# Kernel optimization log

Hardware: AMD Instinct MI355X
Metric: run time of the kernel (lower is better)

## Reference

```python
import jax, jax.numpy as jnp
import numpy as np

B, CIN, COUT, H, W = 2, 128, 128, 128, 256
KH, KW = 3, 3
CMID = 32  # COUT // low_factor


def setup_inputs() -> dict:
    key = jax.random.key(0)
    ks = jax.random.split(key, 7)
    x = jax.random.normal(ks[0], (B, CIN, H, W), jnp.float32)
    # torchvision deform_conv2d offset layout: [2*KH*KW, Ho, Wo], (dy, dx) per tap
    offset = jax.random.normal(ks[1], (2 * KH * KW, H, W), jnp.float32)
    weight = jax.random.normal(ks[2], (COUT, CIN, KH, KW), jnp.float32) * 0.05
    bias = jax.random.normal(ks[3], (COUT,), jnp.float32) * 0.01
    down_w = jax.random.normal(ks[4], (CMID, 2 * COUT), jnp.float32) * 0.05
    up_w = jax.random.normal(ks[5], (COUT, CMID), jnp.float32) * 0.05
    scale = jnp.float32(1.0)
    return dict(x=x, offset=offset, weight=weight, bias=bias,
                down_w=down_w, up_w=up_w, scale=scale)


def _deform_conv2d(x, offset, weight, bias):
    # stride=1, padding=1, dilation=1, groups=1 (matches init_conv config)
    Bn, C, Hh, Ww = x.shape
    Co, _, kh, kw = weight.shape
    K = kh * kw
    Ho, Wo = offset.shape[-2:]
    off = offset.reshape(K, 2, Ho, Wo)
    dy, dx = off[:, 0], off[:, 1]                      # [K, Ho, Wo]
    ki, kj = jnp.meshgrid(jnp.arange(kh), jnp.arange(kw), indexing='ij')
    ki = ki.reshape(K).astype(jnp.float32)
    kj = kj.reshape(K).astype(jnp.float32)
    i = jnp.arange(Ho, dtype=jnp.float32)
    j = jnp.arange(Wo, dtype=jnp.float32)
    PAD = 1.0
    py = i[None, :, None] - PAD + ki[:, None, None] + dy   # [K, Ho, Wo]
    px = j[None, None, :] - PAD + kj[:, None, None] + dx
    y0 = jnp.floor(py).astype(jnp.int32)
    x0 = jnp.floor(px).astype(jnp.int32)
    fy = py - y0.astype(py.dtype)
    fx = px - x0.astype(px.dtype)
    xf = x.reshape(Bn, C, Hh * Ww)

    def gather(yi, xi, w):
        # zero padding outside the image (torchvision semantics)
        valid = (yi >= 0) & (yi < Hh) & (xi >= 0) & (xi < Ww)
        yc = jnp.clip(yi, 0, Hh - 1)
        xc = jnp.clip(xi, 0, Ww - 1)
        idx = (yc * Ww + xc).reshape(-1)                   # [K*Ho*Wo]
        g = xf[:, :, idx].reshape(Bn, C, K, Ho, Wo)
        return g * (w * valid.astype(w.dtype))[None, None]

    val = gather(y0, x0, (1.0 - fy) * (1.0 - fx))
    val = val + gather(y0, x0 + 1, (1.0 - fy) * fx)
    val = val + gather(y0 + 1, x0, fy * (1.0 - fx))
    val = val + gather(y0 + 1, x0 + 1, fy * fx)
    out = jnp.einsum('bcnij,ocn->boij', val, weight.reshape(Co, C, K))
    return out + bias[None, :, None, None]


def reference(x, offset, weight, bias, down_w, up_w, scale):
    # h = original frozen conv (weights shared with the deform branch, ablation != wo_copy)
    h = jax.lax.conv_general_dilated(
        x, weight, window_strides=(1, 1), padding=[(1, 1), (1, 1)],
        dimension_numbers=('NCHW', 'OIHW', 'NCHW'))
    h = h + bias[None, :, None, None]
    dx = _deform_conv2d(x, offset, weight, bias)
    dx = jnp.concatenate([dx, h], axis=1)                  # mix == 'cat'
    lo = jnp.einsum('bcij,dc->bdij', dx, down_w)           # 1x1 conv_down
    up = jnp.einsum('bcij,dc->bdij', lo, up_w)             # 1x1 conv_up
    return h + scale * up
```

## Files before the change

kernel.cpp:

```cpp
#include <hip/hip_runtime.h>
#include <hip/hip_bf16.h>

typedef __attribute__((ext_vector_type(8))) short short8;
typedef __attribute__((ext_vector_type(8))) unsigned short ushort8;
typedef __attribute__((ext_vector_type(4))) float f32x4;
typedef __attribute__((ext_vector_type(4))) int int4v;
typedef __attribute__((ext_vector_type(4))) float float4v;
typedef __attribute__((ext_vector_type(2))) float float2v;
typedef __attribute__((ext_vector_type(4))) unsigned int uint4v;

#define HH 128
#define WW 256
#define CIN_ 128
#define COUT_ 128

__device__ __forceinline__ float bf2f(unsigned short u) {
  return __builtin_bit_cast(float, ((unsigned int)u) << 16);
}
__device__ __forceinline__ unsigned short f2bf(float f) {
  union { __hip_bfloat16 h; unsigned short u; } v;
  v.h = __float2bfloat16(f);
  return v.u;
}

__global__ void k_prep_T(const float* __restrict__ down_w,
                         const float* __restrict__ weight,
                         float* __restrict__ T) {
  int e = blockIdx.x * 256 + threadIdx.x;
  if (e >= 2 * 32 * 1152) return;
  int s = e / 36864, r = e % 36864, d = r / 1152, ck = r % 1152;
  float a = 0.f;
  #pragma unroll 4
  for (int p = 0; p < 128; ++p)
    a += down_w[d * 256 + s * 128 + p] * weight[p * 1152 + ck];
  T[e] = a;
}

__global__ void k_prep_W(const float* __restrict__ up_w,
                         const float* __restrict__ weight,
                         const float* __restrict__ T,
                         const float* __restrict__ scale,
                         unsigned short* __restrict__ wdef,
                         unsigned short* __restrict__ wstd) {
  int e = blockIdx.x * 256 + threadIdx.x;
  if (e >= 2 * 9 * 128 * 128) return;
  int s = e / 147456, r = e % 147456;
  int tap = r / 16384, o = (r / 128) % 128, c = r % 128;
  int ck = c * 9 + tap;
  const float* Ts = T + s * 36864;
  float a = 0.f;
  #pragma unroll
  for (int d = 0; d < 32; ++d) a += up_w[o * 32 + d] * Ts[d * 1152 + ck];
  float scl = scale[0];
  int idx = ((tap * 4 + (c >> 5)) * 128 + o) * 32 + (c & 31);
  if (s == 1) {
    wstd[idx] = f2bf(weight[o * 1152 + ck] + scl * a);
  } else {
    wdef[idx] = f2bf(scl * a);
  }
}

__global__ void k_prep_bias(const float* __restrict__ down_w,
                            const float* __restrict__ up_w,
                            const float* __restrict__ bias,
                            const float* __restrict__ scale,
                            float* __restrict__ beff) {
  __shared__ float sd[32];
  int t = threadIdx.x;
  if (t < 32) {
    float a = 0.f;
    for (int p = 0; p < 128; ++p)
      a += (down_w[t * 256 + p] + down_w[t * 256 + 128 + p]) * bias[p];
    sd[t] = a;
  }
  __syncthreads();
  if (t < 128) {
    float a = 0.f;
    #pragma unroll
    for (int d = 0; d < 32; ++d) a += up_w[t * 32 + d] * sd[d];
    beff[t] = bias[t] + scale[0] * a;
  }
}

__global__ __launch_bounds__(256) void k_nhwc(const float* __restrict__ x,
                                              unsigned short* __restrict__ xh) {
  __shared__ float tile[32 * 129];
  int idx = blockIdx.x;
  int b = idx >> 10, rem = idx & 1023;
  int y = rem >> 3, xg = (rem & 7) << 5;
  int tid = threadIdx.x;
  for (int it = tid; it < 32 * 128; it += 256) {
    int c = it >> 5, xi = it & 31;
    tile[xi * 129 + c] = x[(((size_t)b * 128 + c) * 128 + y) * 256 + xg + xi];
  }
  __syncthreads();
  for (int it = tid; it < 32 * 16; it += 256) {
    int xi = it >> 4, cs = it & 15;
    ushort8 v;
    #pragma unroll
    for (int e = 0; e < 8; ++e) v[e] = f2bf(tile[xi * 129 + cs * 8 + e]);
    *(ushort8*)(xh + (((size_t)b * 128 + y) * 256 + xg + xi) * 128 + cs * 8) = v;
  }
}

__global__ void k_meta(const float* __restrict__ offset,
                       int4v* __restrict__ mo, float4v* __restrict__ mw) {
  int e = blockIdx.x * 256 + threadIdx.x;
  if (e >= 9 * 128 * 256) return;
  int k = e >> 15, rem = e & 32767;
  int ii = rem >> 8, jj = rem & 255;
  float dy = offset[(2 * k) * 32768 + rem];
  float dx = offset[(2 * k + 1) * 32768 + rem];
  int ki = k / 3, kj = k % 3;
  float py = (float)(ii - 1 + ki) + dy;
  float px = (float)(jj - 1 + kj) + dx;
  float fy0 = floorf(py), fx0 = floorf(px);
  int y0 = (int)fy0, x0 = (int)fx0;
  float fy = py - fy0, fx = px - fx0;
  int ys[2] = {y0, y0 + 1};
  int xs_[2] = {x0, x0 + 1};
  float wy[2] = {1.f - fy, fy}, wx[2] = {1.f - fx, fx};
  int4v o;
  float4v w;
  #pragma unroll
  for (int cy = 0; cy < 2; ++cy) {
    #pragma unroll
    for (int cx = 0; cx < 2; ++cx) {
      int yy = ys[cy], xx = xs_[cx];
      bool valid = (yy >= 0) && (yy < HH) && (xx >= 0) && (xx < WW);
      int yc = min(max(yy, 0), HH - 1), xc = min(max(xx, 0), WW - 1);
      int off = (yc * WW + xc) * CIN_;
      float wv = valid ? wy[cy] * wx[cx] : 0.f;
      int ci = cy * 2 + cx;
      if (ci == 0) { o.x = off; w.x = wv; }
      else if (ci == 1) { o.y = off; w.y = wv; }
      else if (ci == 2) { o.z = off; w.z = wv; }
      else { o.w = off; w.w = wv; }
    }
  }
  mo[e] = o;
  mw[e] = w;
}

__global__ __launch_bounds__(256, 4) void k_main(
    const unsigned short* __restrict__ xh,
    const int4v* __restrict__ mo, const float4v* __restrict__ mw,
    const unsigned short* __restrict__ wstd, const unsigned short* __restrict__ wdef,
    const float* __restrict__ beff, float* __restrict__ out) {
  __shared__ __align__(16) unsigned short sbuf[2][64 * 128];

  int t = blockIdx.x;
  int b = t >> 9, i = (t >> 2) & 127, j0 = (t & 3) << 6;
  int tid = threadIdx.x;
  const unsigned short* xb = xh + (size_t)b * (HH * WW * CIN_);

  int slot = tid & 15, pg = tid >> 4;
  int ce = slot * 8;

  int lane = tid & 63, wid = tid >> 6;
  int obase = wid << 5;
  int lrow = lane & 15, lhi = lane >> 4;

  f32x4 acc[2][4] = {};

  auto STAGE_DEF = [&](int tap, unsigned short* buf) {
    int4v o;
    float4v wq0, wq1;
    uint4v g0[4], g1[4];
    int mbase = (tap * HH + i) * WW + j0 + pg;

    o = mo[mbase]; wq0 = mw[mbase];
    g0[0] = *(const uint4v*)(xb + o.x + ce);
    g0[1] = *(const uint4v*)(xb + o.y + ce);
    g0[2] = *(const uint4v*)(xb + o.z + ce);
    g0[3] = *(const uint4v*)(xb + o.w + ce);
    o = mo[mbase + 16]; wq1 = mw[mbase + 16];
    g1[0] = *(const uint4v*)(xb + o.x + ce);
    g1[1] = *(const uint4v*)(xb + o.y + ce);
    g1[2] = *(const uint4v*)(xb + o.z + ce);
    g1[3] = *(const uint4v*)(xb + o.w + ce);

    auto COMB = [&](uint4v* g, float4v w, int q) {
      int p = q * 16 + pg;
      uint4v r;
      #pragma unroll
      for (int wi = 0; wi < 4; ++wi) {
        unsigned u0 = g[0][wi], u1 = g[1][wi], u2 = g[2][wi], u3 = g[3][wi];
        float2v f0 = {__builtin_bit_cast(float, u0 << 16), __builtin_bit_cast(float, u0 & 0xffff0000u)};
        float2v f1 = {__builtin_bit_cast(float, u1 << 16), __builtin_bit_cast(float, u1 & 0xffff0000u)};
        float2v f2 = {__builtin_bit_cast(float, u2 << 16), __builtin_bit_cast(float, u2 & 0xffff0000u)};
        float2v f3 = {__builtin_bit_cast(float, u3 << 16), __builtin_bit_cast(float, u3 & 0xffff0000u)};
        float2v s = w.x * f0 + w.y * f1 + w.z * f2 + w.w * f3;
        r[wi] = (unsigned)f2bf(s.x) | ((unsigned)f2bf(s.y) << 16);
      }
      *(uint4v*)((char*)buf + (p << 8) + ((slot ^ (p & 15)) << 4)) = r;
    };

    COMB(g0, wq0, 0);
    o = mo[mbase + 32]; wq0 = mw[mbase + 32];
    g0[0] = *(const uint4v*)(xb + o.x + ce);
    g0[1] = *(const uint4v*)(xb + o.y + ce);
    g0[2] = *(const uint4v*)(xb + o.z + ce);
    g0[3] = *(const uint4v*)(xb + o.w + ce);
    COMB(g1, wq1, 1);
    o = mo[mbase + 48]; wq1 = mw[mbase + 48];
    g1[0] = *(const uint4v*)(xb + o.x + ce);
    g1[1] = *(const uint4v*)(xb + o.y + ce);
    g1[2] = *(const uint4v*)(xb + o.z + ce);
    g1[3] = *(const uint4v*)(xb + o.w + ce);
    COMB(g0, wq0, 2);
    COMB(g1, wq1, 3);
  };

  auto STAGE_STD = [&](int tap, unsigned short* buf) {
    int ki = tap / 3, kj = tap % 3;
    int gy = i - 1 + ki;
    bool oky = (unsigned)gy < (unsigned)HH;
    uint4v s[4];
    #pragma unroll
    for (int q = 0; q < 4; ++q) {
      int p = q * 16 + pg;
      int gx = j0 + p - 1 + kj;
      uint4v vv = {};
      if (oky && (unsigned)gx < (unsigned)WW)
        vv = *(const uint4v*)(xb + (size_t)(gy * WW + gx) * CIN_ + ce);
      s[q] = vv;
    }
    #pragma unroll
    for (int q = 0; q < 4; ++q) {
      int p = q * 16 + pg;
      *(uint4v*)((char*)buf + (p << 8) + ((slot ^ (p & 15)) << 4)) = s[q];
    }
  };

  auto COMPUTE = [&](int v) {
    const unsigned short* cur = sbuf[v & 1];
    const unsigned short* wt = ((v & 1) ? wdef : wstd) + (size_t)(v >> 1) * 16384;
    #pragma unroll
    for (int cc = 0; cc < 4; ++cc) {
      short8 af[2];
      #pragma unroll
      for (int am = 0; am < 2; ++am)
        af[am] = *(const short8*)(wt + ((size_t)(cc * 128 + obase + am * 16 + lrow)) * 32 + lhi * 8);
      short8 bfr[4];
      #pragma unroll
      for (int bn = 0; bn < 4; ++bn) {
        int pp = bn * 16 + lrow;
        bfr[bn] = *(const short8*)((const char*)cur + (pp << 8) +
                                   (((cc * 4 + lhi) ^ lrow) << 4));
      }
      #pragma unroll
      for (int am = 0; am < 2; ++am)
        #pragma unroll
        for (int bn = 0; bn < 4; ++bn)
          acc[am][bn] = __builtin_amdgcn_mfma_f32_16x16x32_bf16(af[am], bfr[bn], acc[am][bn], 0, 0, 0);
    }
  };

  STAGE_STD(0, sbuf[0]);
  __syncthreads();

  for (int v = 0; v < 18; ++v) {
    if (v < 17) {
      int nv = v + 1;
      if (nv & 1) STAGE_DEF(nv >> 1, sbuf[nv & 1]);
      else        STAGE_STD(nv >> 1, sbuf[nv & 1]);
    }
    COMPUTE(v);
    __syncthreads();
  }

  #pragma unroll
  for (int am = 0; am < 2; ++am) {
    #pragma unroll
    for (int bn = 0; bn < 4; ++bn) {
      int jg = j0 + bn * 16 + lrow;
      #pragma unroll
      for (int r = 0; r < 4; ++r) {
        int o = obase + am * 16 + lhi * 4 + r;
        out[(((size_t)b * COUT_ + o) * HH + i) * WW + jg] = acc[am][bn][r] + beff[o];
      }
    }
  }
}

extern "C" void kernel_launch(void* const* d_in, const int* in_sizes, int n_in,
                              void* d_out, int out_size, void* d_ws, size_t ws_size,
                              hipStream_t stream) {
  const float* x      = (const float*)d_in[0];
  const float* offset = (const float*)d_in[1];
  const float* weight = (const float*)d_in[2];
  const float* bias   = (const float*)d_in[3];
  const float* down_w = (const float*)d_in[4];
  const float* up_w   = (const float*)d_in[5];
  const float* scale  = (const float*)d_in[6];
  float* out = (float*)d_out;

  char* ws = (char*)d_ws;
  unsigned short* xh   = (unsigned short*)(ws);
  int4v* mo            = (int4v*)(ws + 16777216);
  float4v* mw          = (float4v*)(ws + 21495808);
  unsigned short* wstd = (unsigned short*)(ws + 26214400);
  unsigned short* wdef = (unsigned short*)(ws + 26509312);
  float* T             = (float*)(ws + 26804224);
  float* beff          = (float*)(ws + 27099136);

  k_prep_T<<<dim3(288), dim3(256), 0, stream>>>(down_w, weight, T);
  k_prep_W<<<dim3(1152), dim3(256), 0, stream>>>(up_w, weight, T, scale, wdef, wstd);
  k_prep_bias<<<dim3(1), dim3(128), 0, stream>>>(down_w, up_w, bias, scale, beff);
  k_nhwc<<<dim3(2048), dim3(256), 0, stream>>>(x, xh);
  k_meta<<<dim3(1152), dim3(256), 0, stream>>>(offset, mo, mw);
  k_main<<<dim3(1024), dim3(256), 0, stream>>>(xh, mo, mw, wstd, wdef, beff, out);
}
```

Measured before the change: 115.1 us.

## Interleave gather loads with split MFMA compute and remap block order

```diff
diff --git a/kernel.cpp b/kernel.cpp
--- a/kernel.cpp
+++ b/kernel.cpp
@@ -127,7 +127,7 @@
     #pragma unroll
     for (int cx = 0; cx < 2; ++cx) {
       int yy = ys[cy], xx = xs_[cx];
-      bool valid = (yy >= 0) && (yy < HH) && (xx >= 0) && (xx < WW);
+      bool valid = (yy >= 0) && (yy < HH) && (xx < WW) && (xx >= 0);
       int yc = min(max(yy, 0), HH - 1), xc = min(max(xx, 0), WW - 1);
       int off = (yc * WW + xc) * CIN_;
       float wv = valid ? wy[cy] * wx[cx] : 0.f;
@@ -149,7 +149,8 @@
     const float* __restrict__ beff, float* __restrict__ out) {
   __shared__ __align__(16) unsigned short sbuf[2][64 * 128];
 
-  int t = blockIdx.x;
+  int orig = blockIdx.x;
+  int t = ((orig & 7) << 7) + (orig >> 3);
   int b = t >> 9, i = (t >> 2) & 127, j0 = (t & 3) << 6;
   int tid = threadIdx.x;
   const unsigned short* xb = xh + (size_t)b * (HH * WW * CIN_);
@@ -163,56 +164,25 @@
 
   f32x4 acc[2][4] = {};
 
-  auto STAGE_DEF = [&](int tap, unsigned short* buf) {
-    int4v o;
-    float4v wq0, wq1;
-    uint4v g0[4], g1[4];
-    int mbase = (tap * HH + i) * WW + j0 + pg;
-
-    o = mo[mbase]; wq0 = mw[mbase];
-    g0[0] = *(const uint4v*)(xb + o.x + ce);
-    g0[1] = *(const uint4v*)(xb + o.y + ce);
-    g0[2] = *(const uint4v*)(xb + o.z + ce);
-    g0[3] = *(const uint4v*)(xb + o.w + ce);
-    o = mo[mbase + 16]; wq1 = mw[mbase + 16];
-    g1[0] = *(const uint4v*)(xb + o.x + ce);
-    g1[1] = *(const uint4v*)(xb + o.y + ce);
-    g1[2] = *(const uint4v*)(xb + o.z + ce);
-    g1[3] = *(const uint4v*)(xb + o.w + ce);
-
-    auto COMB = [&](uint4v* g, float4v w, int q) {
-      int p = q * 16 + pg;
-      uint4v r;
-      #pragma unroll
-      for (int wi = 0; wi < 4; ++wi) {
-        unsigned u0 = g[0][wi], u1 = g[1][wi], u2 = g[2][wi], u3 = g[3][wi];
-        float2v f0 = {__builtin_bit_cast(float, u0 << 16), __builtin_bit_cast(float, u0 & 0xffff0000u)};
-        float2v f1 = {__builtin_bit_cast(float, u1 << 16), __builtin_bit_cast(float, u1 & 0xffff0000u)};
-        float2v f2 = {__builtin_bit_cast(float, u2 << 16), __builtin_bit_cast(float, u2 & 0xffff0000u)};
-        float2v f3 = {__builtin_bit_cast(float, u3 << 16), __builtin_bit_cast(float, u3 & 0xffff0000u)};
-        float2v s = w.x * f0 + w.y * f1 + w.z * f2 + w.w * f3;
-        r[wi] = (unsigned)f2bf(s.x) | ((unsigned)f2bf(s.y) << 16);
-      }
-      *(uint4v*)((char*)buf + (p << 8) + ((slot ^ (p & 15)) << 4)) = r;
-    };
-
-    COMB(g0, wq0, 0);
-    o = mo[mbase + 32]; wq0 = mw[mbase + 32];
-    g0[0] = *(const uint4v*)(xb + o.x + ce);
-    g0[1] = *(const uint4v*)(xb + o.y + ce);
-    g0[2] = *(const uint4v*)(xb + o.z + ce);
-    g0[3] = *(const uint4v*)(xb + o.w + ce);
-    COMB(g1, wq1, 1);
-    o = mo[mbase + 48]; wq1 = mw[mbase + 48];
-    g1[0] = *(const uint4v*)(xb + o.x + ce);
-    g1[1] = *(const uint4v*)(xb + o.y + ce);
-    g1[2] = *(const uint4v*)(xb + o.z + ce);
-    g1[3] = *(const uint4v*)(xb + o.w + ce);
-    COMB(g0, wq0, 2);
-    COMB(g1, wq1, 3);
+  auto COMB = [&](uint4v* g, float4v w, int q, unsigned short* buf) {
+    int p = q * 16 + pg;
+    uint4v r;
+    #pragma unroll
+    for (int wi = 0; wi < 4; ++wi) {
+      unsigned u0 = g[0][wi], u1 = g[1][wi], u2 = g[2][wi], u3 = g[3][wi];
+      float2v f0 = {__builtin_bit_cast(float, u0 << 16), __builtin_bit_cast(float, u0 & 0xffff0000u)};
+      float2v f1 = {__builtin_bit_cast(float, u1 << 16), __builtin_bit_cast(float, u1 & 0xffff0000u)};
+      float2v f2 = {__builtin_bit_cast(float, u2 << 16), __builtin_bit_cast(float, u2 & 0xffff0000u)};
+      float2v f3 = {__builtin_bit_cast(float, u3 << 16), __builtin_bit_cast(float, u3 & 0xffff0000u)};
+      float2v s = w.x * f0 + w.y * f1 + w.z * f2 + w.w * f3;
+      unsigned rr;
+      asm("v_cvt_pk_bf16_f32 %0, %1, %2" : "=v"(rr) : "v"(s.x), "v"(s.y));
+      r[wi] = rr;
+    }
+    *(uint4v*)((char*)buf + (p << 8) + ((slot ^ (p & 15)) << 4)) = r;
   };
 
-  auto STAGE_STD = [&](int tap, unsigned short* buf) {
+  auto STAGE_STD_FULL = [&](int tap, unsigned short* buf) {
     int ki = tap / 3, kj = tap % 3;
     int gy = i - 1 + ki;
     bool oky = (unsigned)gy < (unsigned)HH;
@@ -233,11 +203,12 @@
     }
   };
 
-  auto COMPUTE = [&](int v) {
+  auto COMPUTE_HALF = [&](int v, int half) {
     const unsigned short* cur = sbuf[v & 1];
     const unsigned short* wt = ((v & 1) ? wdef : wstd) + (size_t)(v >> 1) * 16384;
     #pragma unroll
-    for (int cc = 0; cc < 4; ++cc) {
+    for (int c2 = 0; c2 < 2; ++c2) {
+      int cc = half * 2 + c2;
       short8 af[2];
       #pragma unroll
       for (int am = 0; am < 2; ++am)
@@ -257,16 +228,83 @@
     }
   };
 
-  STAGE_STD(0, sbuf[0]);
+  STAGE_STD_FULL(0, sbuf[0]);
   __syncthreads();
 
   for (int v = 0; v < 18; ++v) {
-    if (v < 17) {
-      int nv = v + 1;
-      if (nv & 1) STAGE_DEF(nv >> 1, sbuf[nv & 1]);
-      else        STAGE_STD(nv >> 1, sbuf[nv & 1]);
-    }
-    COMPUTE(v);
+    int nv = v + 1;
+    if (nv < 18 && (nv & 1)) {
+      int tap = nv >> 1;
+      unsigned short* nb = sbuf[nv & 1];
+      int mbase = (tap * HH + i) * WW + j0 + pg;
+      int4v o0 = mo[mbase], o1 = mo[mbase + 16];
+      float4v w0 = mw[mbase], w1 = mw[mbase + 16];
+      uint4v gA[4], gB[4];
+      gA[0] = *(const uint4v*)(xb + o0.x + ce);
+      gA[1] = *(const uint4v*)(xb + o0.y + ce);
+      gA[2] = *(const uint4v*)(xb + o0.z + ce);
+      gA[3] = *(const uint4v*)(xb + o0.w + ce);
+      gB[0] = *(const uint4v*)(xb + o1.x + ce);
+      gB[1] = *(const uint4v*)(xb + o1.y + ce);
+      gB[2] = *(const uint4v*)(xb + o1.z + ce);
+      gB[3] = *(const uint4v*)(xb + o1.w + ce);
+      __builtin_amdgcn_sched_barrier(0);
+      COMPUTE_HALF(v, 0);
+      __builtin_amdgcn_sched_barrier(0);
+      COMB(gA, w0, 0, nb);
+      int4v o2 = mo[mbase + 32];
+      float4v w2 = mw[mbase + 32];
+      gA[0] = *(const uint4v*)(xb + o2.x + ce);
+      gA[1] = *(const uint4v*)(xb + o2.y + ce);
+      gA[2] = *(const uint4v*)(xb + o2.z + ce);
+      gA[3] = *(const uint4v*)(xb + o2.w + ce);
+      COMB(gB, w1, 1, nb);
+      int4v o3 = mo[mbase + 48];
+      float4v w3 = mw[mbase + 48];
+      gB[0] = *(const uint4v*)(xb + o3.x + ce);
+      gB[1] = *(const uint4v*)(xb + o3.y + ce);
+      gB[2] = *(const uint4v*)(xb + o3.z + ce);
+      gB[3] = *(const uint4v*)(xb + o3.w + ce);
+      __builtin_amdgcn_sched_barrier(0);
+      COMPUTE_HALF(v, 1);
+      __builtin_amdgcn_sched_barrier(0);
+      COMB(gA, w2, 2, nb);
+      COMB(gB, w3, 3, nb);
+    } else if (nv < 18) {
+      int tap = nv >> 1;
+      unsigned short* nb = sbuf[nv & 1];
+      int ki = tap / 3, kj = tap % 3;
+      int gy = i - 1 + ki;
+      bool oky = (unsigned)gy < (unsigned)HH;
+      uint4v s0 = {}, s1 = {}, s2 = {}, s3 = {};
+      {
+        int gx0 = j0 + pg - 1 + kj;
+        int gx1 = gx0 + 16, gx2 = gx0 + 32, gx3 = gx0 + 48;
+        if (oky && (unsigned)gx0 < (unsigned)WW)
+          s0 = *(const uint4v*)(xb + (size_t)(gy * WW + gx0) * CIN_ + ce);
+        if (oky && (unsigned)gx1 < (unsigned)WW)
+          s1 = *(const uint4v*)(xb + (size_t)(gy * WW + gx1) * CIN_ + ce);
+        if (oky && (unsigned)gx2 < (unsigned)WW)
+          s2 = *(const uint4v*)(xb + (size_t)(gy * WW + gx2) * CIN_ + ce);
+        if (oky && (unsigned)gx3 < (unsigned)WW)
+          s3 = *(const uint4v*)(xb + (size_t)(gy * WW + gx3) * CIN_ + ce);
+      }
+      __builtin_amdgcn_sched_barrier(0);
+      COMPUTE_HALF(v, 0);
+      __builtin_amdgcn_sched_barrier(0);
+      {
+        int p0 = pg, p1 = pg + 16, p2 = pg + 32, p3 = pg + 48;
+        *(uint4v*)((char*)nb + (p0 << 8) + ((slot ^ (p0 & 15)) << 4)) = s0;
+        *(uint4v*)((char*)nb + (p1 << 8) + ((slot ^ (p1 & 15)) << 4)) = s1;
+        *(uint4v*)((char*)nb + (p2 << 8) + ((slot ^ (p2 & 15)) << 4)) = s2;
+        *(uint4v*)((char*)nb + (p3 << 8) + ((slot ^ (p3 & 15)) << 4)) = s3;
+      }
+      __builtin_amdgcn_sched_barrier(0);
+      COMPUTE_HALF(v, 1);
+    } else {
+      COMPUTE_HALF(v, 0);
+      COMPUTE_HALF(v, 1);
+    }
     __syncthreads();
   }
 
```

After: 137.3 us. +19.2%, slower.
